# Performance work log

Measured on AMD Instinct MI355X. Metric: run time of the kernel, lower is better.

## Reference

```python
import jax, jax.numpy as jnp
import numpy as np

D_MODEL = 1024
N_HEADS = 16
D_HEAD = D_MODEL // N_HEADS          # 64
FRACTION_TO_ROTATE = 0.25
ROT_DIM = int(FRACTION_TO_ROTATE * D_HEAD)  # 16 (even)
ROPE_BASE = 10000.0


def setup_inputs() -> dict:
    key = jax.random.key(0)
    ks = jax.random.split(key, 10)
    B, S = 2, 2048
    init = lambda k, fan_in, shape: jax.random.normal(k, shape, jnp.float32) / np.sqrt(fan_in)
    return {
        "x": jax.random.normal(ks[0], (B, S, D_MODEL), jnp.float32),
        "Wq": init(ks[1], D_MODEL, (D_MODEL, D_MODEL)),
        "bq": jnp.zeros((D_MODEL,), jnp.float32),
        "Wk": init(ks[2], D_MODEL, (D_MODEL, D_MODEL)),
        "bk": jnp.zeros((D_MODEL,), jnp.float32),
        "Wv": init(ks[3], D_MODEL, (D_MODEL, D_MODEL)),
        "bv": jnp.zeros((D_MODEL,), jnp.float32),
        "Wo": init(ks[4], D_MODEL, (D_MODEL, D_MODEL)),
        "bo": jnp.zeros((D_MODEL,), jnp.float32),
    }


def _apply_partial_rope(t, cos, sin):
    # t: [B, H, S, d_head]; rotate first ROT_DIM dims, pass the rest through.
    rot, rest = t[..., :ROT_DIM], t[..., ROT_DIM:]
    half = ROT_DIM // 2
    t1, t2 = rot[..., :half], rot[..., half:]
    # cos/sin: [S, half] -> broadcast over [B, H]
    r1 = t1 * cos - t2 * sin
    r2 = t1 * sin + t2 * cos
    return jnp.concatenate([r1, r2, rest], axis=-1)


def reference(x, Wq, bq, Wk, bk, Wv, bv, Wo, bo):
    B, S, D = x.shape
    q = (x @ Wq + bq).reshape(B, S, N_HEADS, D_HEAD).transpose(0, 2, 1, 3)
    k = (x @ Wk + bk).reshape(B, S, N_HEADS, D_HEAD).transpose(0, 2, 1, 3)
    v = (x @ Wv + bv).reshape(B, S, N_HEADS, D_HEAD).transpose(0, 2, 1, 3)

    half = ROT_DIM // 2
    inv_freq = 1.0 / (ROPE_BASE ** (jnp.arange(half, dtype=jnp.float32) / half))
    angles = jnp.arange(S, dtype=jnp.float32)[:, None] * inv_freq  # [S, half]
    cos, sin = jnp.cos(angles), jnp.sin(angles)

    q = _apply_partial_rope(q, cos, sin)
    k = _apply_partial_rope(k, cos, sin)

    scale = 1.0 / np.sqrt(D_HEAD).astype(np.float32)
    scores = jnp.einsum("bhqd,bhkd->bhqk", q, k) * scale  # [B,H,S,S]
    causal = jnp.tril(jnp.ones((S, S), dtype=bool))
    scores = jnp.where(causal, scores, jnp.finfo(scores.dtype).min)
    probs = jax.nn.softmax(scores, axis=-1)

    out = jnp.einsum("bhqk,bhkd->bhqd", probs, v)  # [B,H,S,d_head]
    out = out.transpose(0, 2, 1, 3).reshape(B, S, D)
    return out @ Wo + bo
```

## Files before the change

### kernel.cpp

```cpp
#include <hip/hip_runtime.h>
#include <hip/hip_bf16.h>
#include <math.h>

constexpr int DM = 1024;
constexpr int SEQ = 2048;
constexpr int BATCH = 2;
constexpr int NH = 16;
constexpr int DH = 64;
constexpr int MROWS = BATCH * SEQ;
constexpr float SCALE = 0.125f;

typedef __attribute__((ext_vector_type(8))) short short8;
typedef __attribute__((ext_vector_type(4))) float f32x4;
typedef unsigned short ushort_t;

__device__ __forceinline__ unsigned short f2b(float f) {
    __hip_bfloat16 h = __float2bfloat16(f);
    return __builtin_bit_cast(unsigned short, h);
}
__device__ __forceinline__ float b2f(unsigned short u) {
    unsigned int t = ((unsigned int)u) << 16;
    return __builtin_bit_cast(float, t);
}
__device__ __forceinline__ unsigned int cvtpk_bf16(float lo, float hi) {
    unsigned int r;
    asm("v_cvt_pk_bf16_f32 %0, %1, %2" : "=v"(r) : "v"(lo), "v"(hi));
    return r;
}
__device__ __forceinline__ f32x4 mfma16_bf16(uint2 a, uint2 b, f32x4 c) {
    asm("v_mfma_f32_16x16x16_bf16 %0, %1, %2, %0"
        : "+v"(c) : "v"(a), "v"(b));
    return c;
}

__device__ __forceinline__ void gload16(const ushort_t* g, ushort_t* l) {
    __builtin_amdgcn_global_load_lds(
        (const __attribute__((address_space(1))) void*)g,
        (__attribute__((address_space(3))) void*)l, 16, 0, 0);
}

__global__ __launch_bounds__(256) void conv_x(const float* __restrict__ x,
                                              ushort_t* __restrict__ xb) {
    const size_t idx = (size_t)blockIdx.x * 256 + threadIdx.x;
    const float4* src = (const float4*)(x + idx * 8);
    float4 a = src[0], b = src[1];
    short8 v;
    v[0] = (short)f2b(a.x); v[1] = (short)f2b(a.y);
    v[2] = (short)f2b(a.z); v[3] = (short)f2b(a.w);
    v[4] = (short)f2b(b.x); v[5] = (short)f2b(b.y);
    v[6] = (short)f2b(b.z); v[7] = (short)f2b(b.w);
    *(short8*)(xb + idx * 8) = v;
}

__global__ __launch_bounds__(256) void conv_w(
    const float* __restrict__ Wq, const float* __restrict__ Wk,
    const float* __restrict__ Wv, const float* __restrict__ Wo,
    ushort_t* __restrict__ Wqt, ushort_t* __restrict__ Wkt,
    ushort_t* __restrict__ Wvt, ushort_t* __restrict__ Wot) {
    const float* W; ushort_t* Wt;
    switch (blockIdx.z) {
        case 0:  W = Wq; Wt = Wqt; break;
        case 1:  W = Wk; Wt = Wkt; break;
        case 2:  W = Wv; Wt = Wvt; break;
        default: W = Wo; Wt = Wot; break;
    }
    __shared__ float L[64][65];
    const int n0 = blockIdx.x * 64, k0 = blockIdx.y * 64;
    const int t = threadIdx.x;
    const int tr = t >> 4, tc4 = (t & 15) * 4;
#pragma unroll
    for (int i = 0; i < 4; ++i) {
        int kk = tr + i * 16;
        float4 v = *(const float4*)&W[(size_t)(k0 + kk) * DM + n0 + tc4];
        L[kk][tc4 + 0] = v.x; L[kk][tc4 + 1] = v.y;
        L[kk][tc4 + 2] = v.z; L[kk][tc4 + 3] = v.w;
    }
    __syncthreads();
#pragma unroll
    for (int i = 0; i < 4; ++i) {
        int nn = tr + i * 16;
        ushort4 u;
        u.x = f2b(L[tc4 + 0][nn]); u.y = f2b(L[tc4 + 1][nn]);
        u.z = f2b(L[tc4 + 2][nn]); u.w = f2b(L[tc4 + 3][nn]);
        *(ushort4*)&Wt[(size_t)(n0 + nn) * DM + k0 + tc4] = u;
    }
}

#define BM 128
#define BN 128
#define BKK 32
#define NKT (DM / BKK)

__device__ __forceinline__ void stage_tile(const ushort_t* __restrict__ A,
                                           const ushort_t* __restrict__ B,
                                           int row0, int col0, int kt,
                                           ushort_t* As, ushort_t* Bs, int tid) {
#pragma unroll
    for (int i = 0; i < 2; ++i) {
        int f = i * 256 + tid;
        int sr = f >> 3, p = f & 7;
        int u = p ^ (sr & 7);
        int r = 2 * sr + (u >> 2);
        int c = u & 3;
        gload16(&A[(size_t)(row0 + r) * DM + kt * BKK + c * 8], &As[f * 8]);
        gload16(&B[(size_t)(col0 + r) * DM + kt * BKK + c * 8], &Bs[f * 8]);
    }
}

__device__ __forceinline__ void mfma_core(const ushort_t* __restrict__ A,
                                          const ushort_t* __restrict__ B,
                                          int row0, int col0,
                                          ushort_t* smem, f32x4 (&acc)[4][4]) {
    const int tid = threadIdx.x;
    const int wave = tid >> 6, lane = tid & 63;
    const int lg = lane >> 4, ln = lane & 15;
    const int wr = wave >> 1, wc = wave & 1;

    stage_tile(A, B, row0, col0, 0, smem, smem + 4096, tid);
    __builtin_amdgcn_sched_barrier(0);
    stage_tile(A, B, row0, col0, 1, smem + 8192, smem + 12288, tid);

    for (int kt = 0; kt < NKT; ++kt) {
        if (kt + 1 < NKT)
            asm volatile("s_waitcnt vmcnt(4)" ::: "memory");
        else
            asm volatile("s_waitcnt vmcnt(0)" ::: "memory");
        __builtin_amdgcn_s_barrier();

        if (kt + 2 < NKT) {
            ushort_t* An = smem + ((kt + 2) % 3) * 8192;
            stage_tile(A, B, row0, col0, kt + 2, An, An + 4096, tid);
        }

        const ushort_t* As = smem + (kt % 3) * 8192;
        const ushort_t* Bs = As + 4096;
        short8 af[4], bf[4];
#pragma unroll
        for (int mi = 0; mi < 4; ++mi) {
            int r = wr * 64 + mi * 16 + ln;
            int sr = r >> 1;
            int p = (((r & 1) << 2) | lg) ^ (sr & 7);
            af[mi] = *(const short8*)&As[sr * 64 + p * 8];
        }
#pragma unroll
        for (int ni = 0; ni < 4; ++ni) {
            int r = wc * 64 + ni * 16 + ln;
            int sr = r >> 1;
            int p = (((r & 1) << 2) | lg) ^ (sr & 7);
            bf[ni] = *(const short8*)&Bs[sr * 64 + p * 8];
        }
        __builtin_amdgcn_s_setprio(1);
#pragma unroll
        for (int mi = 0; mi < 4; ++mi)
#pragma unroll
            for (int ni = 0; ni < 4; ++ni)
                acc[mi][ni] = __builtin_amdgcn_mfma_f32_16x16x32_bf16(
                    af[mi], bf[ni], acc[mi][ni], 0, 0, 0);
        __builtin_amdgcn_s_setprio(0);
    }
}

__global__ __launch_bounds__(256) void mfma_gemm_qkv(
    const ushort_t* __restrict__ xb,
    const ushort_t* __restrict__ Wqt, const ushort_t* __restrict__ Wkt,
    const ushort_t* __restrict__ Wvt,
    const float* __restrict__ bq, const float* __restrict__ bk,
    const float* __restrict__ bv,
    ushort_t* __restrict__ qb, ushort_t* __restrict__ kb,
    ushort_t* __restrict__ vtb) {
    const ushort_t* W; const float* bias;
    if (blockIdx.z == 0)      { W = Wqt; bias = bq; }
    else if (blockIdx.z == 1) { W = Wkt; bias = bk; }
    else                      { W = Wvt; bias = bv; }

    const int row0 = blockIdx.y * BM;
    const int col0 = blockIdx.x * BN;
    __shared__ ushort_t smem[24576];
    f32x4 acc[4][4] = {};
    mfma_core(xb, W, row0, col0, smem, acc);

    const int tid = threadIdx.x;
    const int wave = tid >> 6, lane = tid & 63;
    const int lg = lane >> 4, ln = lane & 15;
    const int wr = wave >> 1, wc = wave & 1;
    const bool isV = (blockIdx.z == 2);

    __syncthreads();
    ushort_t* Cs = smem;
#pragma unroll
    for (int mi = 0; mi < 4; ++mi)
#pragma unroll
        for (int ni = 0; ni < 4; ++ni)
#pragma unroll
            for (int r = 0; r < 4; ++r) {
                int mrel = wr * 64 + mi * 16 + lg * 4 + r;
                int nrel = wc * 64 + ni * 16 + ln;
                float v = acc[mi][ni][r] + bias[col0 + nrel];
                Cs[isV ? (nrel * 128 + mrel) : (mrel * 128 + nrel)] = f2b(v);
            }
    __syncthreads();

    if (!isV) {
        ushort_t* out = (blockIdx.z == 0) ? qb : kb;
#pragma unroll
        for (int i = 0; i < 8; ++i) {
            int f = i * 256 + tid;
            int rrow = f >> 4, c8 = f & 15;
            int m = row0 + rrow;
            int b = m >> 11, s = m & (SEQ - 1);
            int n = col0 + c8 * 8;
            int h = n >> 6, d = n & 63;
            short8 val;
            if (d < 16) {
                const ushort_t* base = &Cs[rrow * 128 + (c8 & 8) * 8];
                const bool hi = (d >= 8);
#pragma unroll
                for (int j = 0; j < 8; ++j) {
                    float t1 = b2f(base[j]);
                    float t2 = b2f(base[8 + j]);
                    float invf = __expf(-(float)j * 1.1512925465f);
                    float ang = (float)s * invf;
                    float c_, si_;
                    __sincosf(ang, &si_, &c_);
                    val[j] = (short)f2b(hi ? (t1 * si_ + t2 * c_)
                                           : (t1 * c_ - t2 * si_));
                }
            } else {
                val = *(const short8*)&Cs[rrow * 128 + c8 * 8];
            }
            *(short8*)&out[((size_t)((b * NH + h) * SEQ) + s) * DH + d] = val;
        }
    } else {
#pragma unroll
        for (int i = 0; i < 8; ++i) {
            int f = i * 256 + tid;
            int nrow = f >> 4, c8 = f & 15;
            int n = col0 + nrow;
            int h = n >> 6, d = n & 63;
            int m = row0 + c8 * 8;
            int b = m >> 11, s = m & (SEQ - 1);
            *(short8*)&vtb[((size_t)((b * NH + h) * DH) + d) * SEQ + s] =
                *(const short8*)&Cs[nrow * 128 + c8 * 8];
        }
    }
}

__global__ __launch_bounds__(256) void mfma_gemm_out(
    const ushort_t* __restrict__ ctxb, const ushort_t* __restrict__ Wot,
    const float* __restrict__ bo, float* __restrict__ out) {
    const int row0 = blockIdx.y * BM;
    const int col0 = blockIdx.x * BN;
    __shared__ ushort_t smem[24576];
    f32x4 acc[4][4] = {};
    mfma_core(ctxb, Wot, row0, col0, smem, acc);

    const int tid = threadIdx.x;
    const int wave = tid >> 6, lane = tid & 63;
    const int lg = lane >> 4, ln = lane & 15;
    const int wr = wave >> 1, wc = wave & 1;
#pragma unroll
    for (int mi = 0; mi < 4; ++mi)
#pragma unroll
        for (int ni = 0; ni < 4; ++ni)
#pragma unroll
            for (int r = 0; r < 4; ++r) {
                int m = row0 + wr * 64 + mi * 16 + lg * 4 + r;
                int n = col0 + wc * 64 + ni * 16 + ln;
                out[(size_t)m * DM + n] = acc[mi][ni][r] + bo[n];
            }
}

#define AQT 64
#define AKT 64
#define NQT (SEQ / AQT)

__global__ __launch_bounds__(256) void attn_mfma(
    const ushort_t* __restrict__ qb, const ushort_t* __restrict__ kb,
    const ushort_t* __restrict__ vtb, ushort_t* __restrict__ ctxb,
    ushort_t* __restrict__ opart, float* __restrict__ lpart) {
    constexpr float C1 = 0.18033688f;
    constexpr float M2 = 1.44269504f;
    const int bh = blockIdx.x;
    const int y = blockIdx.y;

    int qt, t0, t1, chunk;
    if (y < 16)      { qt = 16 + y;  t0 = 0;  t1 = 16;     chunk = 0; }
    else if (y < 32) { qt = 47 - y;  t0 = 16; t1 = qt + 1; chunk = 1; }
    else             { qt = 47 - y;  t0 = 0;  t1 = qt + 1; chunk = -1; }
    const int q0 = qt * AQT;

    const int tid = threadIdx.x;
    const int wave = tid >> 6;
    const int lane = tid & 63;
    const int lg = lane >> 4;
    const int ln = lane & 15;

    __shared__ ushort_t KT[2][64 * 64];
    __shared__ ushort_t VT[2][64 * 64];

    const ushort_t* kbase = kb + (size_t)bh * SEQ * DH;
    const ushort_t* vbase = vtb + (size_t)bh * DH * SEQ;
    const int b = bh >> 4, h = bh & 15;

    const ushort_t* qrow = qb + ((size_t)bh * SEQ + q0 + wave * 16 + ln) * DH;
    short8 qf0 = *(const short8*)&qrow[lg * 8];
    short8 qf1 = *(const short8*)&qrow[32 + lg * 8];

    f32x4 o[4];
#pragma unroll
    for (int nt = 0; nt < 4; nt++) o[nt] = f32x4{0.f, 0.f, 0.f, 0.f};
    float l = 0.f;

#pragma unroll
    for (int i = 0; i < 2; i++) {
        int f = i * 256 + tid;
        int r = f >> 3, p = f & 7, c = p ^ (r & 7);
        gload16(&kbase[(size_t)(t0 * AKT + r) * DH + c * 8], &KT[0][f * 8]);
        gload16(&vbase[(size_t)r * SEQ + t0 * AKT + c * 8], &VT[0][f * 8]);
    }

    int cur = 0;
    for (int t = t0; t < t1; ++t) {
        __syncthreads();

        if (t + 1 < t1) {
            const int nb0 = (t + 1) * AKT;
            const int nxt = cur ^ 1;
#pragma unroll
            for (int i = 0; i < 2; i++) {
                int f = i * 256 + tid;
                int r = f >> 3, p = f & 7, c = p ^ (r & 7);
                gload16(&kbase[(size_t)(nb0 + r) * DH + c * 8], &KT[nxt][f * 8]);
                gload16(&vbase[(size_t)r * SEQ + nb0 + c * 8], &VT[nxt][f * 8]);
            }
        }

        float st[4][4];
        __builtin_amdgcn_s_setprio(1);
#pragma unroll
        for (int kt = 0; kt < 4; kt++) {
            f32x4 acc = f32x4{0.f, 0.f, 0.f, 0.f};
            int krow = kt * 16 + ln;
            short8 b0 = *(const short8*)&KT[cur][krow * 64 + ((lg ^ (krow & 7)) * 8)];
            short8 b1 = *(const short8*)&KT[cur][krow * 64 + (((4 + lg) ^ (krow & 7)) * 8)];
            acc = __builtin_amdgcn_mfma_f32_16x16x32_bf16(b0, qf0, acc, 0, 0, 0);
            acc = __builtin_amdgcn_mfma_f32_16x16x32_bf16(b1, qf1, acc, 0, 0, 0);
#pragma unroll
            for (int r = 0; r < 4; r++) st[kt][r] = acc[r];
        }
        __builtin_amdgcn_s_setprio(0);

        if (t == qt) {
            const int qrel = wave * 16 + ln;
#pragma unroll
            for (int kt = 0; kt < 4; kt++)
#pragma unroll
                for (int r = 0; r < 4; r++)
                    if (kt * 16 + lg * 4 + r > qrel) st[kt][r] = -1e30f;
        }

        uint2 pkq[4];
#pragma unroll
        for (int kt = 0; kt < 4; kt++) {
            float pv[4];
#pragma unroll
            for (int r = 0; r < 4; r++) {
                pv[r] = exp2f(fmaf(C1, st[kt][r], -M2));
                l += pv[r];
            }
            pkq[kt].x = cvtpk_bf16(pv[0], pv[1]);
            pkq[kt].y = cvtpk_bf16(pv[2], pv[3]);
        }

        __builtin_amdgcn_s_setprio(1);
#pragma unroll
        for (int nt = 0; nt < 4; nt++) {
            int vrow = nt * 16 + ln;
#pragma unroll
            for (int kt = 0; kt < 4; kt++) {
                int chunk16 = (2 * kt + (lg >> 1)) ^ (vrow & 7);
                uint2 vb = *(const uint2*)&VT[cur][vrow * 64 + chunk16 * 8 + (lg & 1) * 4];
                o[nt] = mfma16_bf16(pkq[kt], vb, o[nt]);
            }
        }
        __builtin_amdgcn_s_setprio(0);

        cur ^= 1;
    }

    l += __shfl_xor(l, 16);
    l += __shfl_xor(l, 32);

    if (chunk >= 0) {
        const int pid = ((bh << 4) + (qt - 16)) * 2 + chunk;
        if (lg == 0) lpart[pid * 64 + wave * 16 + ln] = l;
        ushort_t* ob = opart + (size_t)pid * 4096;
#pragma unroll
        for (int r = 0; r < 4; r++) {
            int qrel = wave * 16 + lg * 4 + r;
#pragma unroll
            for (int nt = 0; nt < 4; nt++)
                ob[qrel * 64 + nt * 16 + ln] = f2b(o[nt][r]);
        }
    } else {
        const float rcp = 1.f / l;
#pragma unroll
        for (int r = 0; r < 4; r++) {
            float invl = __shfl(rcp, (lane & 48) | (lg * 4 + r));
            int qg = q0 + wave * 16 + lg * 4 + r;
            ushort_t* op = ctxb + ((size_t)(b * SEQ + qg)) * DM + h * DH;
#pragma unroll
            for (int nt = 0; nt < 4; nt++)
                op[nt * 16 + ln] = f2b(o[nt][r] * invl);
        }
    }
}

__global__ __launch_bounds__(256) void attn_reduce(
    const ushort_t* __restrict__ opart, const float* __restrict__ lpart,
    ushort_t* __restrict__ ctxb) {
    const int bh = blockIdx.x;
    const int qt = 16 + blockIdx.y;
    const int tid = threadIdx.x;
    const int q = tid >> 2;
    const int d0 = (tid & 3) * 16;

    const int pid0 = ((bh << 4) + (qt - 16)) * 2;
    const ushort_t* o0 = opart + (size_t)pid0 * 4096 + q * 64 + d0;
    const ushort_t* o1 = opart + (size_t)(pid0 + 1) * 4096 + q * 64 + d0;
    const float inv = 1.f / (lpart[pid0 * 64 + q] + lpart[(pid0 + 1) * 64 + q]);

    const int b = bh >> 4, h = bh & 15;
    ushort_t* op = ctxb + ((size_t)(b * SEQ + qt * 64 + q)) * DM + h * DH + d0;
#pragma unroll
    for (int half = 0; half < 2; ++half) {
        short8 a = *(const short8*)&o0[half * 8];
        short8 c = *(const short8*)&o1[half * 8];
        short8 r;
#pragma unroll
        for (int j = 0; j < 8; ++j)
            r[j] = (short)f2b((b2f((unsigned short)a[j]) +
                               b2f((unsigned short)c[j])) * inv);
        *(short8*)&op[half * 8] = r;
    }
}

extern "C" void kernel_launch(void* const* d_in, const int* in_sizes, int n_in,
                              void* d_out, int out_size, void* d_ws, size_t ws_size,
                              hipStream_t stream) {
    const float* x  = (const float*)d_in[0];
    const float* Wq = (const float*)d_in[1];
    const float* bq = (const float*)d_in[2];
    const float* Wk = (const float*)d_in[3];
    const float* bk = (const float*)d_in[4];
    const float* Wv = (const float*)d_in[5];
    const float* bv = (const float*)d_in[6];
    const float* Wo = (const float*)d_in[7];
    const float* bo = (const float*)d_in[8];
    float* out = (float*)d_out;

    constexpr size_t TSZ = (size_t)MROWS * DM;
    constexpr size_t WSZ = (size_t)DM * DM;
    ushort_t* xb  = (ushort_t*)d_ws;
    ushort_t* Wqt = xb + TSZ;
    ushort_t* Wkt = Wqt + WSZ;
    ushort_t* Wvt = Wkt + WSZ;
    ushort_t* Wot = Wvt + WSZ;
    ushort_t* qbp = Wot + WSZ;
    ushort_t* kbp = qbp + TSZ;
    ushort_t* vtp = kbp + TSZ;
    ushort_t* ctxb = vtp + TSZ;

    ushort_t* opart = xb;
    float* lpart = (float*)Wqt;

    conv_x<<<TSZ / 8 / 256, 256, 0, stream>>>(x, xb);
    conv_w<<<dim3(16, 16, 4), 256, 0, stream>>>(Wq, Wk, Wv, Wo, Wqt, Wkt, Wvt, Wot);

    mfma_gemm_qkv<<<dim3(DM / BN, MROWS / BM, 3), 256, 0, stream>>>(
        xb, Wqt, Wkt, Wvt, bq, bk, bv, qbp, kbp, vtp);

    attn_mfma<<<dim3(BATCH * NH, 48), 256, 0, stream>>>(
        qbp, kbp, vtp, ctxb, opart, lpart);
    attn_reduce<<<dim3(BATCH * NH, 16), 256, 0, stream>>>(opart, lpart, ctxb);

    mfma_gemm_out<<<dim3(DM / BN, MROWS / BM), 256, 0, stream>>>(ctxb, Wot, bo, out);
}
```

Before: 116.3 us.

## Process 128-query tiles per attention block to reuse K/V tiles

Each attention block now handles two 64-row query sub-tiles (128 queries) and shares each loaded K/V tile in shared memory between them. Causal masking, the split-KV partitioning and the reduce kernel are reworked to match the 128-row tiles, and the grid is halved. This halves K/V global loads per query and doubles MFMA work per sync, at the cost of more registers per thread, fewer blocks to fill the GPU, and some wasted MFMA work on the diagonal tiles.

```diff
diff --git a/kernel.cpp b/kernel.cpp
--- a/kernel.cpp
+++ b/kernel.cpp
@@ -270,9 +270,7 @@
             }
 }
 
-#define AQT 64
 #define AKT 64
-#define NQT (SEQ / AQT)
 
 __global__ __launch_bounds__(256) void attn_mfma(
     const ushort_t* __restrict__ qb, const ushort_t* __restrict__ kb,
@@ -283,11 +281,11 @@
     const int bh = blockIdx.x;
     const int y = blockIdx.y;
 
-    int qt, t0, t1, chunk;
-    if (y < 16)      { qt = 16 + y;  t0 = 0;  t1 = 16;     chunk = 0; }
-    else if (y < 32) { qt = 47 - y;  t0 = 16; t1 = qt + 1; chunk = 1; }
-    else             { qt = 47 - y;  t0 = 0;  t1 = qt + 1; chunk = -1; }
-    const int q0 = qt * AQT;
+    int t128, t0, t1, chunk;
+    if (y < 8)       { t128 = 8 + y;  t0 = 0;  t1 = 16;           chunk = 0; }
+    else if (y < 16) { t128 = 23 - y; t0 = 16; t1 = 2 * t128 + 2; chunk = 1; }
+    else             { t128 = 23 - y; t0 = 0;  t1 = 2 * t128 + 2; chunk = -1; }
+    const int q0 = t128 * 128;
 
     const int tid = threadIdx.x;
     const int wave = tid >> 6;
@@ -302,14 +300,20 @@
     const ushort_t* vbase = vtb + (size_t)bh * DH * SEQ;
     const int b = bh >> 4, h = bh & 15;
 
-    const ushort_t* qrow = qb + ((size_t)bh * SEQ + q0 + wave * 16 + ln) * DH;
-    short8 qf0 = *(const short8*)&qrow[lg * 8];
-    short8 qf1 = *(const short8*)&qrow[32 + lg * 8];
-
-    f32x4 o[4];
-#pragma unroll
-    for (int nt = 0; nt < 4; nt++) o[nt] = f32x4{0.f, 0.f, 0.f, 0.f};
-    float l = 0.f;
+    const ushort_t* qr0 = qb + ((size_t)bh * SEQ + q0 + wave * 16 + ln) * DH;
+    const ushort_t* qr1 = qr0 + (size_t)64 * DH;
+    short8 q00 = *(const short8*)&qr0[lg * 8];
+    short8 q01 = *(const short8*)&qr0[32 + lg * 8];
+    short8 q10 = *(const short8*)&qr1[lg * 8];
+    short8 q11 = *(const short8*)&qr1[32 + lg * 8];
+
+    f32x4 o0[4], o1[4];
+#pragma unroll
+    for (int nt = 0; nt < 4; nt++) {
+        o0[nt] = f32x4{0.f, 0.f, 0.f, 0.f};
+        o1[nt] = f32x4{0.f, 0.f, 0.f, 0.f};
+    }
+    float l0 = 0.f, l1 = 0.f;
 
 #pragma unroll
     for (int i = 0; i < 2; i++) {
@@ -320,11 +324,11 @@
     }
 
     int cur = 0;
-    for (int t = t0; t < t1; ++t) {
+    for (int j = t0; j < t1; ++j) {
         __syncthreads();
 
-        if (t + 1 < t1) {
-            const int nb0 = (t + 1) * AKT;
+        if (j + 1 < t1) {
+            const int nb0 = (j + 1) * AKT;
             const int nxt = cur ^ 1;
 #pragma unroll
             for (int i = 0; i < 2; i++) {
@@ -335,41 +339,51 @@
             }
         }
 
-        float st[4][4];
+        float st0[4][4], st1[4][4];
         __builtin_amdgcn_s_setprio(1);
 #pragma unroll
         for (int kt = 0; kt < 4; kt++) {
-            f32x4 acc = f32x4{0.f, 0.f, 0.f, 0.f};
             int krow = kt * 16 + ln;
             short8 b0 = *(const short8*)&KT[cur][krow * 64 + ((lg ^ (krow & 7)) * 8)];
             short8 b1 = *(const short8*)&KT[cur][krow * 64 + (((4 + lg) ^ (krow & 7)) * 8)];
-            acc = __builtin_amdgcn_mfma_f32_16x16x32_bf16(b0, qf0, acc, 0, 0, 0);
-            acc = __builtin_amdgcn_mfma_f32_16x16x32_bf16(b1, qf1, acc, 0, 0, 0);
-#pragma unroll
-            for (int r = 0; r < 4; r++) st[kt][r] = acc[r];
+            f32x4 a0 = f32x4{0.f, 0.f, 0.f, 0.f};
+            a0 = __builtin_amdgcn_mfma_f32_16x16x32_bf16(b0, q00, a0, 0, 0, 0);
+            a0 = __builtin_amdgcn_mfma_f32_16x16x32_bf16(b1, q01, a0, 0, 0, 0);
+            f32x4 a1 = f32x4{0.f, 0.f, 0.f, 0.f};
+            a1 = __builtin_amdgcn_mfma_f32_16x16x32_bf16(b0, q10, a1, 0, 0, 0);
+            a1 = __builtin_amdgcn_mfma_f32_16x16x32_bf16(b1, q11, a1, 0, 0, 0);
+#pragma unroll
+            for (int r = 0; r < 4; r++) { st0[kt][r] = a0[r]; st1[kt][r] = a1[r]; }
         }
         __builtin_amdgcn_s_setprio(0);
 
-        if (t == qt) {
-            const int qrel = wave * 16 + ln;
+        if (j >= 2 * t128) {
+            const int kb128 = (j - 2 * t128) * 64;
+            const int qq = wave * 16 + ln;
 #pragma unroll
             for (int kt = 0; kt < 4; kt++)
 #pragma unroll
-                for (int r = 0; r < 4; r++)
-                    if (kt * 16 + lg * 4 + r > qrel) st[kt][r] = -1e30f;
-        }
-
-        uint2 pkq[4];
+                for (int r = 0; r < 4; r++) {
+                    int key = kb128 + kt * 16 + lg * 4 + r;
+                    if (key > qq) st0[kt][r] = -1e30f;
+                    if (key > 64 + qq) st1[kt][r] = -1e30f;
+                }
+        }
+
+        uint2 pk0[4], pk1[4];
 #pragma unroll
         for (int kt = 0; kt < 4; kt++) {
-            float pv[4];
+            float p0[4], p1[4];
 #pragma unroll
             for (int r = 0; r < 4; r++) {
-                pv[r] = exp2f(fmaf(C1, st[kt][r], -M2));
-                l += pv[r];
-            }
-            pkq[kt].x = cvtpk_bf16(pv[0], pv[1]);
-            pkq[kt].y = cvtpk_bf16(pv[2], pv[3]);
+                p0[r] = exp2f(fmaf(C1, st0[kt][r], -M2));
+                p1[r] = exp2f(fmaf(C1, st1[kt][r], -M2));
+                l0 += p0[r]; l1 += p1[r];
+            }
+            pk0[kt].x = cvtpk_bf16(p0[0], p0[1]);
+            pk0[kt].y = cvtpk_bf16(p0[2], p0[3]);
+            pk1[kt].x = cvtpk_bf16(p1[0], p1[1]);
+            pk1[kt].y = cvtpk_bf16(p1[2], p1[3]);
         }
 
         __builtin_amdgcn_s_setprio(1);
@@ -378,9 +392,10 @@
             int vrow = nt * 16 + ln;
 #pragma unroll
             for (int kt = 0; kt < 4; kt++) {
-                int chunk16 = (2 * kt + (lg >> 1)) ^ (vrow & 7);
-                uint2 vb = *(const uint2*)&VT[cur][vrow * 64 + chunk16 * 8 + (lg & 1) * 4];
-                o[nt] = mfma16_bf16(pkq[kt], vb, o[nt]);
+                int c16 = (2 * kt + (lg >> 1)) ^ (vrow & 7);
+                uint2 vb = *(const uint2*)&VT[cur][vrow * 64 + c16 * 8 + (lg & 1) * 4];
+                o0[nt] = mfma16_bf16(pk0[kt], vb, o0[nt]);
+                o1[nt] = mfma16_bf16(pk1[kt], vb, o1[nt]);
             }
         }
         __builtin_amdgcn_s_setprio(0);
@@ -388,30 +403,39 @@
         cur ^= 1;
     }
 
-    l += __shfl_xor(l, 16);
-    l += __shfl_xor(l, 32);
+    l0 += __shfl_xor(l0, 16); l0 += __shfl_xor(l0, 32);
+    l1 += __shfl_xor(l1, 16); l1 += __shfl_xor(l1, 32);
 
     if (chunk >= 0) {
-        const int pid = ((bh << 4) + (qt - 16)) * 2 + chunk;
-        if (lg == 0) lpart[pid * 64 + wave * 16 + ln] = l;
-        ushort_t* ob = opart + (size_t)pid * 4096;
+        const int pid = ((bh << 3) + (t128 - 8)) * 2 + chunk;
+        if (lg == 0) {
+            lpart[pid * 128 + wave * 16 + ln] = l0;
+            lpart[pid * 128 + 64 + wave * 16 + ln] = l1;
+        }
+        ushort_t* ob = opart + (size_t)pid * 8192;
 #pragma unroll
         for (int r = 0; r < 4; r++) {
-            int qrel = wave * 16 + lg * 4 + r;
-#pragma unroll
-            for (int nt = 0; nt < 4; nt++)
-                ob[qrel * 64 + nt * 16 + ln] = f2b(o[nt][r]);
+            int qa = wave * 16 + lg * 4 + r;
+#pragma unroll
+            for (int nt = 0; nt < 4; nt++) {
+                ob[qa * 64 + nt * 16 + ln] = f2b(o0[nt][r]);
+                ob[(64 + qa) * 64 + nt * 16 + ln] = f2b(o1[nt][r]);
+            }
         }
     } else {
-        const float rcp = 1.f / l;
+        const float r0 = 1.f / l0, r1 = 1.f / l1;
 #pragma unroll
         for (int r = 0; r < 4; r++) {
-            float invl = __shfl(rcp, (lane & 48) | (lg * 4 + r));
-            int qg = q0 + wave * 16 + lg * 4 + r;
-            ushort_t* op = ctxb + ((size_t)(b * SEQ + qg)) * DM + h * DH;
-#pragma unroll
-            for (int nt = 0; nt < 4; nt++)
-                op[nt * 16 + ln] = f2b(o[nt][r] * invl);
+            float i0 = __shfl(r0, (lane & 48) | (lg * 4 + r));
+            float i1 = __shfl(r1, (lane & 48) | (lg * 4 + r));
+            int qg0 = q0 + wave * 16 + lg * 4 + r;
+            ushort_t* p0 = ctxb + ((size_t)(b * SEQ + qg0)) * DM + h * DH;
+            ushort_t* p1 = ctxb + ((size_t)(b * SEQ + qg0 + 64)) * DM + h * DH;
+#pragma unroll
+            for (int nt = 0; nt < 4; nt++) {
+                p0[nt * 16 + ln] = f2b(o0[nt][r] * i0);
+                p1[nt * 16 + ln] = f2b(o1[nt][r] * i1);
+            }
         }
     }
 }
@@ -420,28 +444,28 @@
     const ushort_t* __restrict__ opart, const float* __restrict__ lpart,
     ushort_t* __restrict__ ctxb) {
     const int bh = blockIdx.x;
-    const int qt = 16 + blockIdx.y;
+    const int t128 = 8 + blockIdx.y;
     const int tid = threadIdx.x;
-    const int q = tid >> 2;
-    const int d0 = (tid & 3) * 16;
-
-    const int pid0 = ((bh << 4) + (qt - 16)) * 2;
-    const ushort_t* o0 = opart + (size_t)pid0 * 4096 + q * 64 + d0;
-    const ushort_t* o1 = opart + (size_t)(pid0 + 1) * 4096 + q * 64 + d0;
-    const float inv = 1.f / (lpart[pid0 * 64 + q] + lpart[(pid0 + 1) * 64 + q]);
+    const int q = tid >> 1;
+    const int d0 = (tid & 1) * 32;
+
+    const int pid0 = ((bh << 3) + (t128 - 8)) * 2;
+    const ushort_t* o0 = opart + (size_t)pid0 * 8192 + q * 64 + d0;
+    const ushort_t* o1 = opart + (size_t)(pid0 + 1) * 8192 + q * 64 + d0;
+    const float inv = 1.f / (lpart[pid0 * 128 + q] + lpart[(pid0 + 1) * 128 + q]);
 
     const int b = bh >> 4, h = bh & 15;
-    ushort_t* op = ctxb + ((size_t)(b * SEQ + qt * 64 + q)) * DM + h * DH + d0;
-#pragma unroll
-    for (int half = 0; half < 2; ++half) {
-        short8 a = *(const short8*)&o0[half * 8];
-        short8 c = *(const short8*)&o1[half * 8];
+    ushort_t* op = ctxb + ((size_t)(b * SEQ + t128 * 128 + q)) * DM + h * DH + d0;
+#pragma unroll
+    for (int c = 0; c < 4; ++c) {
+        short8 a = *(const short8*)&o0[c * 8];
+        short8 d = *(const short8*)&o1[c * 8];
         short8 r;
 #pragma unroll
         for (int j = 0; j < 8; ++j)
             r[j] = (short)f2b((b2f((unsigned short)a[j]) +
-                               b2f((unsigned short)c[j])) * inv);
-        *(short8*)&op[half * 8] = r;
+                               b2f((unsigned short)d[j])) * inv);
+        *(short8*)&op[c * 8] = r;
     }
 }
 
@@ -480,9 +504,9 @@
     mfma_gemm_qkv<<<dim3(DM / BN, MROWS / BM, 3), 256, 0, stream>>>(
         xb, Wqt, Wkt, Wvt, bq, bk, bv, qbp, kbp, vtp);
 
-    attn_mfma<<<dim3(BATCH * NH, 48), 256, 0, stream>>>(
+    attn_mfma<<<dim3(BATCH * NH, 24), 256, 0, stream>>>(
         qbp, kbp, vtp, ctxb, opart, lpart);
-    attn_reduce<<<dim3(BATCH * NH, 16), 256, 0, stream>>>(opart, lpart, ctxb);
+    attn_reduce<<<dim3(BATCH * NH, 8), 256, 0, stream>>>(opart, lpart, ctxb);
 
     mfma_gemm_out<<<dim3(DM / BN, MROWS / BM), 256, 0, stream>>>(ctxb, Wot, bo, out);
 }
```

Result: slower. 119.4 us (+2.7%).
